# Optimization experiments

Measured on AMD Instinct MI355X. Metric: run time of the kernel, lower is better.

## Reference

```python
import jax, jax.numpy as jnp
import numpy as np

B, T, I, C, O = 256, 1024, 128, 256, 10


def setup_inputs() -> dict:
    key = jax.random.key(0)
    k1, k2, k3, k4, k5 = jax.random.split(key, 5)
    x = jax.random.normal(k1, (B, T, I), dtype=jnp.float32)
    # xavier-like scale for kernels
    kernel = jax.random.normal(k2, (I, 2 * C), dtype=jnp.float32) * (6.0 / (I + 2 * C)) ** 0.5
    recurrent_kernel = jax.random.normal(k3, (C, 2 * C), dtype=jnp.float32) * (6.0 / (C + 2 * C)) ** 0.5
    # bias: forget-gate half initialized to log(uniform(1, T-1)), rest zero
    u = jax.random.uniform(k4, (C,), minval=1.0, maxval=float(T - 1))
    recurrent_bias = jnp.concatenate([jnp.log(u), jnp.zeros((C,), jnp.float32)])
    dense_w = jax.random.normal(k5, (C, O), dtype=jnp.float32) * (1.0 / C) ** 0.5
    dense_b = jnp.zeros((O,), jnp.float32)
    return {"x": x, "kernel": kernel, "recurrent_kernel": recurrent_kernel,
            "recurrent_bias": recurrent_bias, "dense_w": dense_w, "dense_b": dense_b}


def reference(x, kernel, recurrent_kernel, recurrent_bias, dense_w, dense_b):
    cells = recurrent_kernel.shape[0]
    # Precompute input projection for all timesteps in one big GEMM: [B,T,2C]
    xz = jnp.einsum('bti,ig->btg', x, kernel) + recurrent_bias
    xz_t = jnp.swapaxes(xz, 0, 1)  # [T, B, 2C] for scan over time

    def step(carry, z_in):
        h, c = carry
        z = z_in + h @ recurrent_kernel  # [B, 2C]
        f = jax.nn.sigmoid(z[:, :cells])
        c_new = f * c + (1.0 - f) * jnp.tanh(z[:, cells:])
        return (c_new, c_new), None

    h0 = jnp.zeros((x.shape[0], cells), x.dtype)
    (h_final, _), _ = jax.lax.scan(step, (h0, h0), xz_t)
    return h_final @ dense_w + dense_b
```

## Files before the change

### kernel.cpp

```cpp
#include <hip/hip_runtime.h>

#define BB 256
#define TT 1024
#define II 128
#define GG 512
#define CC 256
#define L2E 1.44269504f

typedef _Float16 f16;
typedef _Float16 h8_t __attribute__((ext_vector_type(8)));
typedef float f4_t __attribute__((ext_vector_type(4)));
typedef unsigned short ushort_t;
typedef unsigned short us4_t __attribute__((ext_vector_type(4)));

static __device__ __forceinline__ float fast_rcp(float x) {
#if __has_builtin(__builtin_amdgcn_rcpf)
    return __builtin_amdgcn_rcpf(x);
#else
    return 1.f / x;
#endif
}
static __device__ __forceinline__ float fast_exp2(float x) {
#if __has_builtin(__builtin_amdgcn_exp2f)
    return __builtin_amdgcn_exp2f(x);
#else
    return exp2f(x);
#endif
}

__global__ void kt_transpose(const float* __restrict__ kin, f16* __restrict__ kt) {
    int idx = blockIdx.x * 256 + threadIdx.x;
    int k = idx >> 9;
    int n = idx & 511;
    kt[n * II + k] = (f16)kin[k * GG + n];
}

__global__ __launch_bounds__(512, 2)
void gemm_xz(const float* __restrict__ x, const f16* __restrict__ kt,
             const float* __restrict__ bias, ushort_t* __restrict__ xz) {
    const long mtile = blockIdx.x;
    const int wave = threadIdx.x >> 6;
    const int lane = threadIdx.x & 63;
    const int wm = (wave & 1) * 64;
    const int wn = (wave >> 1) * 128;
    const int lm = lane & 15;
    const int q  = lane >> 4;

    f4_t acc[4][8];
#pragma unroll
    for (int mi = 0; mi < 4; ++mi)
#pragma unroll
        for (int nj = 0; nj < 8; ++nj)
            acc[mi][nj] = (f4_t){0.f, 0.f, 0.f, 0.f};

#pragma unroll
    for (int kc = 0; kc < 4; ++kc) {
        h8_t a[4], bf[8];
#pragma unroll
        for (int mi = 0; mi < 4; ++mi) {
            const int rowm = (int)(mtile * 128) + wm + mi * 16 + lm;
            const int b  = rowm & 255;
            const int tt = rowm >> 8;
            const float* ap = x + (size_t)b * (TT * II) + (size_t)tt * II + kc * 32 + q * 8;
            f4_t p0 = *(const f4_t*)ap;
            f4_t p1 = *(const f4_t*)(ap + 4);
            h8_t tv;
            tv[0] = (f16)p0[0]; tv[1] = (f16)p0[1]; tv[2] = (f16)p0[2]; tv[3] = (f16)p0[3];
            tv[4] = (f16)p1[0]; tv[5] = (f16)p1[1]; tv[6] = (f16)p1[2]; tv[7] = (f16)p1[3];
            a[mi] = tv;
        }
#pragma unroll
        for (int nj = 0; nj < 8; ++nj) {
            const f16* bp = kt + (size_t)(wn + nj * 16 + lm) * II + kc * 32 + q * 8;
            bf[nj] = *(const h8_t*)bp;
        }
#pragma unroll
        for (int mi = 0; mi < 4; ++mi)
#pragma unroll
            for (int nj = 0; nj < 8; ++nj)
                acc[mi][nj] = __builtin_amdgcn_mfma_f32_16x16x32_f16(a[mi], bf[nj], acc[mi][nj], 0, 0, 0);
    }

#pragma unroll
    for (int mi = 0; mi < 4; ++mi) {
        const int rowm0 = (int)(mtile * 128) + wm + mi * 16 + q * 4;
        const int t  = rowm0 >> 8;
        const int b0 = rowm0 & 255;
        const int gq = b0 >> 4;
#pragma unroll
        for (int nj = 0; nj < 8; ++nj) {
            const int col = wn + nj * 16 + lm;
            const float bv = bias[col];
            const float s  = (col < CC) ? L2E : (2.0f * L2E);
            us4_t v;
#pragma unroll
            for (int r = 0; r < 4; ++r) {
                f16 hv = (f16)((acc[mi][nj][r] + bv) * s);
                v[r] = *(ushort_t*)&hv;
            }
            *(us4_t*)(xz + (((size_t)t * 16 + gq) * 512 + col) * 16 + q * 4) = v;
        }
    }
}

#define STEP(T, PF, PP, HRD, HWR) do {                                               \
    h8_t af[8];                                                                      \
    _Pragma("unroll") for (int kt = 0; kt < 4; ++kt)                                 \
        af[kt] = *(const h8_t*)((HRD) + lm * 264 + kt * 32 + q * 8);                 \
    f4_t acc[4];                                                                     \
    _Pragma("unroll") for (int ni = 0; ni < 4; ++ni) {                               \
        f4_t av;                                                                     \
        _Pragma("unroll") for (int r = 0; r < 4; ++r) {                              \
            ushort_t u = (PF)[ni * 4 + r];                                           \
            f16 hv = *(f16*)&u;                                                      \
            av[r] = (float)hv;                                                       \
        }                                                                            \
        acc[ni] = av;                                                                \
    }                                                                                \
    if ((T) + 2 < TT) {                                                              \
        _Pragma("unroll") for (int ni = 0; ni < 4; ++ni) {                           \
            us4_t v = *(const us4_t*)((PP) + ni * 2048);                             \
            (PF)[ni * 4 + 0] = v[0];                                                 \
            (PF)[ni * 4 + 1] = v[1];                                                 \
            (PF)[ni * 4 + 2] = v[2];                                                 \
            (PF)[ni * 4 + 3] = v[3];                                                 \
        }                                                                            \
        (PP) += 2 * 131072;                                                          \
    }                                                                                \
                                                  \
    _Pragma("unroll") for (int kt = 0; kt < 4; ++kt) {                               \
        acc[0] = __builtin_amdgcn_mfma_f32_16x16x32_f16(af[kt], bw[0][kt], acc[0], 0, 0, 0); \
        acc[2] = __builtin_amdgcn_mfma_f32_16x16x32_f16(af[kt], bw[2][kt], acc[2], 0, 0, 0); \
    }                                                                                \
    _Pragma("unroll") for (int kt = 0; kt < 4; ++kt) {                               \
        acc[1] = __builtin_amdgcn_mfma_f32_16x16x32_f16(af[kt], bw[1][kt], acc[1], 0, 0, 0); \
        acc[3] = __builtin_amdgcn_mfma_f32_16x16x32_f16(af[kt], bw[3][kt], acc[3], 0, 0, 0); \
    }                                                                                \
    asm volatile("s_waitcnt lgkmcnt(0)\n\ts_barrier" ::: "memory");       \
    _Pragma("unroll") for (int kt = 4; kt < 8; ++kt)                                 \
        af[kt] = *(const h8_t*)((HRD) + lm * 264 + kt * 32 + q * 8);                 \
         \
    _Pragma("unroll") for (int kt = 4; kt < 8; ++kt) {                               \
        acc[0] = __builtin_amdgcn_mfma_f32_16x16x32_f16(af[kt], bw[0][kt], acc[0], 0, 0, 0); \
        acc[2] = __builtin_amdgcn_mfma_f32_16x16x32_f16(af[kt], bw[2][kt], acc[2], 0, 0, 0); \
    }                                                                                \
    _Pragma("unroll") for (int kt = 4; kt < 8; ++kt) {                               \
        acc[1] = __builtin_amdgcn_mfma_f32_16x16x32_f16(af[kt], bw[1][kt], acc[1], 0, 0, 0); \
        acc[3] = __builtin_amdgcn_mfma_f32_16x16x32_f16(af[kt], bw[3][kt], acc[3], 0, 0, 0); \
    }                                                                                \
                                         \
    _Pragma("unroll") for (int r = 0; r < 4; ++r) {                                  \
        float zf = acc[0][r];                                                        \
        float zg = acc[2][r];                                                        \
        float ef = fast_exp2(-zf);                                                   \
        float eg = fast_exp2(-fabsf(zg));                                            \
        float t1 = (zg < 0.f) ? -ef : ef;                                            \
        float cv = cst[0][r];                                                        \
        float num = fmaf(cv, eg, cv) + fmaf(-t1, eg, t1);                            \
        float den = (1.f + ef) * (1.f + eg);                                         \
        cst[0][r] = num * fast_rcp(den);                                             \
        (HWR)[(q * 4 + r) * 264 + wave * 16 + lm] = (f16)cst[0][r];                  \
    }                                                                                \
    asm volatile("s_waitcnt lgkmcnt(0)\n\ts_barrier" ::: "memory");       \
          \
    _Pragma("unroll") for (int r = 0; r < 4; ++r) {                                  \
        float zf = acc[1][r];                                                        \
        float zg = acc[3][r];                                                        \
        float ef = fast_exp2(-zf);                                                   \
        float eg = fast_exp2(-fabsf(zg));                                            \
        float t1 = (zg < 0.f) ? -ef : ef;                                            \
        float cv = cst[1][r];                                                        \
        float num = fmaf(cv, eg, cv) + fmaf(-t1, eg, t1);                            \
        float den = (1.f + ef) * (1.f + eg);                                         \
        cst[1][r] = num * fast_rcp(den);                                             \
        (HWR)[(q * 4 + r) * 264 + (wave + 8) * 16 + lm] = (f16)cst[1][r];            \
    }                                                                                \
} while (0)

__global__ __launch_bounds__(512, 2)
void janet_rec(const float* __restrict__ rk, const float* __restrict__ dw,
               const float* __restrict__ db, const ushort_t* __restrict__ xz,
               float* __restrict__ out) {
    const int g = blockIdx.x;
    const int tid = threadIdx.x;
    const int wave = tid >> 6;
    const int lane = tid & 63;
    const int lm = lane & 15;
    const int q  = lane >> 4;

    h8_t bw[4][8];
#pragma unroll
    for (int ni = 0; ni < 4; ++ni) {
        const float s = (ni < 2) ? L2E : (2.0f * L2E);
#pragma unroll
        for (int kt = 0; kt < 8; ++kt) {
            h8_t tv;
#pragma unroll
            for (int j = 0; j < 8; ++j)
                tv[j] = (f16)(s * rk[(size_t)(kt * 32 + q * 8 + j) * GG + (wave + 8 * ni) * 16 + lm]);
            bw[ni][kt] = tv;
        }
    }

    __shared__ __align__(16) f16 hb[2][16][264];
    f16* h0 = &hb[0][0][0];
    f16* h1 = &hb[1][0][0];
    for (int i = tid; i < 2 * 16 * 264; i += 512) ((f16*)hb)[i] = (f16)0.f;

    float cst[2][4];
#pragma unroll
    for (int ni = 0; ni < 2; ++ni)
#pragma unroll
        for (int r = 0; r < 4; ++r) cst[ni][r] = 0.f;

    const ushort_t* PB = xz + (size_t)g * 8192 + (wave * 16 + lm) * 16 + q * 4;
    const ushort_t* p0 = PB + 2 * 131072;
    const ushort_t* p1 = PB + 3 * 131072;

    ushort_t pf0[16], pf1[16];
#pragma unroll
    for (int ni = 0; ni < 4; ++ni) {
        us4_t v0 = *(const us4_t*)(PB + ni * 2048);
        us4_t v1 = *(const us4_t*)(PB + 131072 + ni * 2048);
        pf0[ni * 4 + 0] = v0[0]; pf0[ni * 4 + 1] = v0[1];
        pf0[ni * 4 + 2] = v0[2]; pf0[ni * 4 + 3] = v0[3];
        pf1[ni * 4 + 0] = v1[0]; pf1[ni * 4 + 1] = v1[1];
        pf1[ni * 4 + 2] = v1[2]; pf1[ni * 4 + 3] = v1[3];
    }
    __syncthreads();

#pragma unroll 1
    for (int t = 0; t < TT; t += 2) {
        STEP(t,     pf0, p0, h0, h1);
        STEP(t + 1, pf1, p1, h1, h0);
    }

    __shared__ float hf[16][256];
#pragma unroll
    for (int ni = 0; ni < 2; ++ni)
#pragma unroll
        for (int r = 0; r < 4; ++r)
            hf[q * 4 + r][(wave + 8 * ni) * 16 + lm] = cst[ni][r];
    __syncthreads();
    if (tid < 160) {
        const int bi = tid / 10, o = tid % 10;
        float acc = db[o];
#pragma unroll 8
        for (int cc = 0; cc < CC; ++cc) acc = fmaf(hf[bi][cc], dw[cc * 10 + o], acc);
        out[(g * 16 + bi) * 10 + o] = acc;
    }
}

__global__ void ws_too_small(float* out, float wssz) {
    int i = blockIdx.x * 256 + threadIdx.x;
    if (i < BB * 10) out[i] = (i == 0) ? wssz : 0.f;
}

extern "C" void kernel_launch(void* const* d_in, const int* in_sizes, int n_in,
                              void* d_out, int out_size, void* d_ws, size_t ws_size,
                              hipStream_t stream) {
    const float* x   = (const float*)d_in[0];
    const float* kin = (const float*)d_in[1];
    const float* rk  = (const float*)d_in[2];
    const float* rb  = (const float*)d_in[3];
    const float* dw  = (const float*)d_in[4];
    const float* db  = (const float*)d_in[5];
    float* out = (float*)d_out;

    const size_t xz_bytes = (size_t)BB * TT * GG * 2;
    const size_t kt_bytes = (size_t)GG * II * 2;
    if (ws_size < xz_bytes + kt_bytes) {
        ws_too_small<<<10, 256, 0, stream>>>(out, (float)ws_size);
        return;
    }

    ushort_t* xz = (ushort_t*)d_ws;
    f16* kt = (f16*)((char*)d_ws + xz_bytes);

    kt_transpose<<<256, 256, 0, stream>>>(kin, kt);
    gemm_xz<<<2048, 512, 0, stream>>>(x, kt, rb, xz);
    janet_rec<<<16, 512, 0, stream>>>(rk, dw, db, xz, out);
}
```

Before: 1.464 ms.

## Fuse input GEMM and recurrence into one launch with per-tile readiness flags

Merges the input-projection GEMM and the recurrent scan into a single kernel. The first 16 blocks run the recurrence and the remaining 2048 blocks compute xz tiles, each publishing a release flag when its tile is written. Recurrence blocks spin on the flags for the timestep they need before prefetching, so the serial scan can start while the GEMM is still running instead of waiting for the whole GEMM to finish. This adds atomic polling overhead. It also relies on the 16 recurrence blocks being scheduled alongside the GEMM blocks, and the extra dynamic shared memory lowers occupancy for the GEMM blocks.

Measured after the change: 1.630 ms. +11.3%, slower.

```diff
diff --git a/kernel.cpp b/kernel.cpp
--- a/kernel.cpp
+++ b/kernel.cpp
@@ -28,79 +28,14 @@
 #endif
 }
 
+__device__ unsigned g_flags[2049];
+
 __global__ void kt_transpose(const float* __restrict__ kin, f16* __restrict__ kt) {
     int idx = blockIdx.x * 256 + threadIdx.x;
+    if (idx < 2049) g_flags[idx] = 0u;
     int k = idx >> 9;
     int n = idx & 511;
     kt[n * II + k] = (f16)kin[k * GG + n];
-}
-
-__global__ __launch_bounds__(512, 2)
-void gemm_xz(const float* __restrict__ x, const f16* __restrict__ kt,
-             const float* __restrict__ bias, ushort_t* __restrict__ xz) {
-    const long mtile = blockIdx.x;
-    const int wave = threadIdx.x >> 6;
-    const int lane = threadIdx.x & 63;
-    const int wm = (wave & 1) * 64;
-    const int wn = (wave >> 1) * 128;
-    const int lm = lane & 15;
-    const int q  = lane >> 4;
-
-    f4_t acc[4][8];
-#pragma unroll
-    for (int mi = 0; mi < 4; ++mi)
-#pragma unroll
-        for (int nj = 0; nj < 8; ++nj)
-            acc[mi][nj] = (f4_t){0.f, 0.f, 0.f, 0.f};
-
-#pragma unroll
-    for (int kc = 0; kc < 4; ++kc) {
-        h8_t a[4], bf[8];
-#pragma unroll
-        for (int mi = 0; mi < 4; ++mi) {
-            const int rowm = (int)(mtile * 128) + wm + mi * 16 + lm;
-            const int b  = rowm & 255;
-            const int tt = rowm >> 8;
-            const float* ap = x + (size_t)b * (TT * II) + (size_t)tt * II + kc * 32 + q * 8;
-            f4_t p0 = *(const f4_t*)ap;
-            f4_t p1 = *(const f4_t*)(ap + 4);
-            h8_t tv;
-            tv[0] = (f16)p0[0]; tv[1] = (f16)p0[1]; tv[2] = (f16)p0[2]; tv[3] = (f16)p0[3];
-            tv[4] = (f16)p1[0]; tv[5] = (f16)p1[1]; tv[6] = (f16)p1[2]; tv[7] = (f16)p1[3];
-            a[mi] = tv;
-        }
-#pragma unroll
-        for (int nj = 0; nj < 8; ++nj) {
-            const f16* bp = kt + (size_t)(wn + nj * 16 + lm) * II + kc * 32 + q * 8;
-            bf[nj] = *(const h8_t*)bp;
-        }
-#pragma unroll
-        for (int mi = 0; mi < 4; ++mi)
-#pragma unroll
-            for (int nj = 0; nj < 8; ++nj)
-                acc[mi][nj] = __builtin_amdgcn_mfma_f32_16x16x32_f16(a[mi], bf[nj], acc[mi][nj], 0, 0, 0);
-    }
-
-#pragma unroll
-    for (int mi = 0; mi < 4; ++mi) {
-        const int rowm0 = (int)(mtile * 128) + wm + mi * 16 + q * 4;
-        const int t  = rowm0 >> 8;
-        const int b0 = rowm0 & 255;
-        const int gq = b0 >> 4;
-#pragma unroll
-        for (int nj = 0; nj < 8; ++nj) {
-            const int col = wn + nj * 16 + lm;
-            const float bv = bias[col];
-            const float s  = (col < CC) ? L2E : (2.0f * L2E);
-            us4_t v;
-#pragma unroll
-            for (int r = 0; r < 4; ++r) {
-                f16 hv = (f16)((acc[mi][nj][r] + bv) * s);
-                v[r] = *(ushort_t*)&hv;
-            }
-            *(us4_t*)(xz + (((size_t)t * 16 + gq) * 512 + col) * 16 + q * 4) = v;
-        }
-    }
 }
 
 #define STEP(T, PF, PP, HRD, HWR) do {                                               \
@@ -118,6 +53,20 @@
         acc[ni] = av;                                                                \
     }                                                                                \
     if ((T) + 2 < TT) {                                                              \
+        if (!alldone) {                                                              \
+            unsigned cn = __hip_atomic_load(&g_flags[2048], __ATOMIC_ACQUIRE,        \
+                                            __HIP_MEMORY_SCOPE_AGENT);               \
+            if (cn == 2048u) { alldone = true; }                                     \
+            else {                                                                   \
+                unsigned ff;                                                         \
+                do {                                                                 \
+                    ff = __hip_atomic_load(&g_flags[2 * ((T) + 2) + gh],             \
+                                           __ATOMIC_ACQUIRE,                         \
+                                           __HIP_MEMORY_SCOPE_AGENT);                \
+                    if (!ff) __builtin_amdgcn_s_sleep(8);                            \
+                } while (!ff);                                                       \
+            }                                                                        \
+        }                                                                            \
         _Pragma("unroll") for (int ni = 0; ni < 4; ++ni) {                           \
             us4_t v = *(const us4_t*)((PP) + ni * 2048);                             \
             (PF)[ni * 4 + 0] = v[0];                                                 \
@@ -178,16 +127,89 @@
 } while (0)
 
 __global__ __launch_bounds__(512, 2)
-void janet_rec(const float* __restrict__ rk, const float* __restrict__ dw,
-               const float* __restrict__ db, const ushort_t* __restrict__ xz,
-               float* __restrict__ out) {
-    const int g = blockIdx.x;
+void janet_fused(const float* __restrict__ x, const f16* __restrict__ kt,
+                 const float* __restrict__ bias, ushort_t* __restrict__ xz,
+                 const float* __restrict__ rk, const float* __restrict__ dw,
+                 const float* __restrict__ db, float* __restrict__ out) {
     const int tid = threadIdx.x;
     const int wave = tid >> 6;
     const int lane = tid & 63;
     const int lm = lane & 15;
     const int q  = lane >> 4;
 
+    if (blockIdx.x >= 16) {
+        const long mtile = blockIdx.x - 16;
+        const int wm = (wave & 1) * 64;
+        const int wn = (wave >> 1) * 128;
+
+        f4_t acc[4][8];
+#pragma unroll
+        for (int mi = 0; mi < 4; ++mi)
+#pragma unroll
+            for (int nj = 0; nj < 8; ++nj)
+                acc[mi][nj] = (f4_t){0.f, 0.f, 0.f, 0.f};
+
+#pragma unroll
+        for (int kc = 0; kc < 4; ++kc) {
+            h8_t a[4], bf[8];
+#pragma unroll
+            for (int mi = 0; mi < 4; ++mi) {
+                const int rowm = (int)(mtile * 128) + wm + mi * 16 + lm;
+                const int b  = rowm & 255;
+                const int tt = rowm >> 8;
+                const float* ap = x + (size_t)b * (TT * II) + (size_t)tt * II + kc * 32 + q * 8;
+                f4_t p0 = *(const f4_t*)ap;
+                f4_t p1 = *(const f4_t*)(ap + 4);
+                h8_t tv;
+                tv[0] = (f16)p0[0]; tv[1] = (f16)p0[1]; tv[2] = (f16)p0[2]; tv[3] = (f16)p0[3];
+                tv[4] = (f16)p1[0]; tv[5] = (f16)p1[1]; tv[6] = (f16)p1[2]; tv[7] = (f16)p1[3];
+                a[mi] = tv;
+            }
+#pragma unroll
+            for (int nj = 0; nj < 8; ++nj) {
+                const f16* bp = kt + (size_t)(wn + nj * 16 + lm) * II + kc * 32 + q * 8;
+                bf[nj] = *(const h8_t*)bp;
+            }
+#pragma unroll
+            for (int mi = 0; mi < 4; ++mi)
+#pragma unroll
+                for (int nj = 0; nj < 8; ++nj)
+                    acc[mi][nj] = __builtin_amdgcn_mfma_f32_16x16x32_f16(a[mi], bf[nj], acc[mi][nj], 0, 0, 0);
+        }
+
+#pragma unroll
+        for (int mi = 0; mi < 4; ++mi) {
+            const int rowm0 = (int)(mtile * 128) + wm + mi * 16 + q * 4;
+            const int t  = rowm0 >> 8;
+            const int b0 = rowm0 & 255;
+            const int gq = b0 >> 4;
+#pragma unroll
+            for (int nj = 0; nj < 8; ++nj) {
+                const int col = wn + nj * 16 + lm;
+                const float bv = bias[col];
+                const float s  = (col < CC) ? L2E : (2.0f * L2E);
+                us4_t v;
+#pragma unroll
+                for (int r = 0; r < 4; ++r) {
+                    f16 hv = (f16)((acc[mi][nj][r] + bv) * s);
+                    v[r] = *(ushort_t*)&hv;
+                }
+                *(us4_t*)(xz + (((size_t)t * 16 + gq) * 512 + col) * 16 + q * 4) = v;
+            }
+        }
+
+        __syncthreads();
+        if (tid == 0) {
+            __hip_atomic_store(&g_flags[(int)mtile], 1u, __ATOMIC_RELEASE, __HIP_MEMORY_SCOPE_AGENT);
+            __hip_atomic_fetch_add(&g_flags[2048], 1u, __ATOMIC_RELEASE, __HIP_MEMORY_SCOPE_AGENT);
+        }
+        return;
+    }
+
+    const int g = blockIdx.x;
+    const int gh = g >> 3;
+    bool alldone = false;
+
     h8_t bw[4][8];
 #pragma unroll
     for (int ni = 0; ni < 4; ++ni) {
@@ -212,6 +234,14 @@
     for (int ni = 0; ni < 2; ++ni)
 #pragma unroll
         for (int r = 0; r < 4; ++r) cst[ni][r] = 0.f;
+
+    {
+        unsigned ff;
+        do { ff = __hip_atomic_load(&g_flags[gh], __ATOMIC_ACQUIRE, __HIP_MEMORY_SCOPE_AGENT);
+             if (!ff) __builtin_amdgcn_s_sleep(8); } while (!ff);
+        do { ff = __hip_atomic_load(&g_flags[2 + gh], __ATOMIC_ACQUIRE, __HIP_MEMORY_SCOPE_AGENT);
+             if (!ff) __builtin_amdgcn_s_sleep(8); } while (!ff);
+    }
 
     const ushort_t* PB = xz + (size_t)g * 8192 + (wave * 16 + lm) * 16 + q * 4;
     const ushort_t* p0 = PB + 2 * 131072;
@@ -278,6 +308,5 @@
     f16* kt = (f16*)((char*)d_ws + xz_bytes);
 
     kt_transpose<<<256, 256, 0, stream>>>(kin, kt);
-    gemm_xz<<<2048, 512, 0, stream>>>(x, kt, rb, xz);
-    janet_rec<<<16, 512, 0, stream>>>(rk, dw, db, xz, out);
-}
+    janet_fused<<<2064, 512, 49152, stream>>>(x, kt, rb, xz, rk, dw, db, out);
+}
```

## Stage x tile in LDS for input GEMM and cut recurrent barriers to one per step

Applied to the files above, without the earlier changes.

The input-projection GEMM now remaps each block to one timestep and 128 batch rows. It loads that x tile once into shared memory as f16 and has the MFMA waves read their A fragments from LDS instead of issuing strided global loads per wave. In the recurrent kernel, each step used to have two barriers with the h-fragment loads split around them. It now loads all eight h fragments up front, runs all MFMAs, and uses a single barrier at the end of the step. The prefetch buffer is also repacked as 32-bit words so loads and converts are cheaper. The main aim is to take barrier latency off the serial 1024-step critical path. The single barrier relies on the double-buffered h arrays for correctness.

New measurement: 1.428 ms. 2.5% less time.

```diff
diff --git a/kernel.cpp b/kernel.cpp
--- a/kernel.cpp
+++ b/kernel.cpp
@@ -9,9 +9,12 @@
 
 typedef _Float16 f16;
 typedef _Float16 h8_t __attribute__((ext_vector_type(8)));
+typedef _Float16 h4_t __attribute__((ext_vector_type(4)));
+typedef _Float16 h2_t __attribute__((ext_vector_type(2)));
 typedef float f4_t __attribute__((ext_vector_type(4)));
 typedef unsigned short ushort_t;
 typedef unsigned short us4_t __attribute__((ext_vector_type(4)));
+typedef unsigned u2_t __attribute__((ext_vector_type(2)));
 
 static __device__ __forceinline__ float fast_rcp(float x) {
 #if __has_builtin(__builtin_amdgcn_rcpf)
@@ -38,13 +41,35 @@
 __global__ __launch_bounds__(512, 2)
 void gemm_xz(const float* __restrict__ x, const f16* __restrict__ kt,
              const float* __restrict__ bias, ushort_t* __restrict__ xz) {
+    const int tid = threadIdx.x;
+    const int wave = tid >> 6;
+    const int lane = tid & 63;
+    const int lm = lane & 15;
+    const int q  = lane >> 4;
+
     const long mtile = blockIdx.x;
-    const int wave = threadIdx.x >> 6;
-    const int lane = threadIdx.x & 63;
     const int wm = (wave & 1) * 64;
     const int wn = (wave >> 1) * 128;
-    const int lm = lane & 15;
-    const int q  = lane >> 4;
+
+    const int tt0 = (int)(mtile >> 1);
+    const int bb0 = ((int)mtile & 1) * 128;
+
+    __shared__ __align__(16) f16 xs[128][132];
+
+    {
+        const int r0  = tid >> 5;
+        const int c16 = tid & 31;
+        const float* xb = x + (size_t)tt0 * II + (size_t)c16 * 4;
+#pragma unroll
+        for (int j = 0; j < 8; ++j) {
+            const int row = r0 + j * 16;
+            f4_t p = *(const f4_t*)(xb + (size_t)(bb0 + row) * (TT * II));
+            h4_t hv;
+            hv[0] = (f16)p[0]; hv[1] = (f16)p[1]; hv[2] = (f16)p[2]; hv[3] = (f16)p[3];
+            *(h4_t*)(&xs[row][c16 * 4]) = hv;
+        }
+    }
+    __syncthreads();
 
     f4_t acc[4][8];
 #pragma unroll
@@ -57,18 +82,8 @@
     for (int kc = 0; kc < 4; ++kc) {
         h8_t a[4], bf[8];
 #pragma unroll
-        for (int mi = 0; mi < 4; ++mi) {
-            const int rowm = (int)(mtile * 128) + wm + mi * 16 + lm;
-            const int b  = rowm & 255;
-            const int tt = rowm >> 8;
-            const float* ap = x + (size_t)b * (TT * II) + (size_t)tt * II + kc * 32 + q * 8;
-            f4_t p0 = *(const f4_t*)ap;
-            f4_t p1 = *(const f4_t*)(ap + 4);
-            h8_t tv;
-            tv[0] = (f16)p0[0]; tv[1] = (f16)p0[1]; tv[2] = (f16)p0[2]; tv[3] = (f16)p0[3];
-            tv[4] = (f16)p1[0]; tv[5] = (f16)p1[1]; tv[6] = (f16)p1[2]; tv[7] = (f16)p1[3];
-            a[mi] = tv;
-        }
+        for (int mi = 0; mi < 4; ++mi)
+            a[mi] = *(const h8_t*)(&xs[wm + mi * 16 + lm][kc * 32 + q * 8]);
 #pragma unroll
         for (int nj = 0; nj < 8; ++nj) {
             const f16* bp = kt + (size_t)(wn + nj * 16 + lm) * II + kc * 32 + q * 8;
@@ -83,10 +98,8 @@
 
 #pragma unroll
     for (int mi = 0; mi < 4; ++mi) {
-        const int rowm0 = (int)(mtile * 128) + wm + mi * 16 + q * 4;
-        const int t  = rowm0 >> 8;
-        const int b0 = rowm0 & 255;
-        const int gq = b0 >> 4;
+        const int b0r = bb0 + wm + mi * 16 + q * 4;
+        const int gq = b0r >> 4;
 #pragma unroll
         for (int nj = 0; nj < 8; ++nj) {
             const int col = wn + nj * 16 + lm;
@@ -98,57 +111,40 @@
                 f16 hv = (f16)((acc[mi][nj][r] + bv) * s);
                 v[r] = *(ushort_t*)&hv;
             }
-            *(us4_t*)(xz + (((size_t)t * 16 + gq) * 512 + col) * 16 + q * 4) = v;
+            *(us4_t*)(xz + (((size_t)tt0 * 16 + gq) * 512 + col) * 16 + q * 4) = v;
         }
     }
 }
 
 #define STEP(T, PF, PP, HRD, HWR) do {                                               \
     h8_t af[8];                                                                      \
-    _Pragma("unroll") for (int kt = 0; kt < 4; ++kt)                                 \
+    _Pragma("unroll") for (int kt = 0; kt < 8; ++kt)                                 \
         af[kt] = *(const h8_t*)((HRD) + lm * 264 + kt * 32 + q * 8);                 \
     f4_t acc[4];                                                                     \
     _Pragma("unroll") for (int ni = 0; ni < 4; ++ni) {                               \
-        f4_t av;                                                                     \
-        _Pragma("unroll") for (int r = 0; r < 4; ++r) {                              \
-            ushort_t u = (PF)[ni * 4 + r];                                           \
-            f16 hv = *(f16*)&u;                                                      \
-            av[r] = (float)hv;                                                       \
-        }                                                                            \
-        acc[ni] = av;                                                                \
+        h2_t a01 = *(h2_t*)&(PF)[ni * 2];                                            \
+        h2_t a23 = *(h2_t*)&(PF)[ni * 2 + 1];                                        \
+        acc[ni] = (f4_t){(float)a01[0], (float)a01[1], (float)a23[0], (float)a23[1]};\
     }                                                                                \
     if ((T) + 2 < TT) {                                                              \
         _Pragma("unroll") for (int ni = 0; ni < 4; ++ni) {                           \
-            us4_t v = *(const us4_t*)((PP) + ni * 2048);                             \
-            (PF)[ni * 4 + 0] = v[0];                                                 \
-            (PF)[ni * 4 + 1] = v[1];                                                 \
-            (PF)[ni * 4 + 2] = v[2];                                                 \
-            (PF)[ni * 4 + 3] = v[3];                                                 \
+            u2_t v = *(const u2_t*)((PP) + ni * 2048);                               \
+            (PF)[ni * 2] = v[0];                                                     \
+            (PF)[ni * 2 + 1] = v[1];                                                 \
         }                                                                            \
         (PP) += 2 * 131072;                                                          \
     }                                                                                \
-                                                  \
-    _Pragma("unroll") for (int kt = 0; kt < 4; ++kt) {                               \
+                                                              \
+    _Pragma("unroll") for (int kt = 0; kt < 8; ++kt) {                               \
         acc[0] = __builtin_amdgcn_mfma_f32_16x16x32_f16(af[kt], bw[0][kt], acc[0], 0, 0, 0); \
         acc[2] = __builtin_amdgcn_mfma_f32_16x16x32_f16(af[kt], bw[2][kt], acc[2], 0, 0, 0); \
     }                                                                                \
-    _Pragma("unroll") for (int kt = 0; kt < 4; ++kt) {                               \
+                                                              \
+    _Pragma("unroll") for (int kt = 0; kt < 8; ++kt) {                               \
         acc[1] = __builtin_amdgcn_mfma_f32_16x16x32_f16(af[kt], bw[1][kt], acc[1], 0, 0, 0); \
         acc[3] = __builtin_amdgcn_mfma_f32_16x16x32_f16(af[kt], bw[3][kt], acc[3], 0, 0, 0); \
     }                                                                                \
-    asm volatile("s_waitcnt lgkmcnt(0)\n\ts_barrier" ::: "memory");       \
-    _Pragma("unroll") for (int kt = 4; kt < 8; ++kt)                                 \
-        af[kt] = *(const h8_t*)((HRD) + lm * 264 + kt * 32 + q * 8);                 \
-         \
-    _Pragma("unroll") for (int kt = 4; kt < 8; ++kt) {                               \
-        acc[0] = __builtin_amdgcn_mfma_f32_16x16x32_f16(af[kt], bw[0][kt], acc[0], 0, 0, 0); \
-        acc[2] = __builtin_amdgcn_mfma_f32_16x16x32_f16(af[kt], bw[2][kt], acc[2], 0, 0, 0); \
-    }                                                                                \
-    _Pragma("unroll") for (int kt = 4; kt < 8; ++kt) {                               \
-        acc[1] = __builtin_amdgcn_mfma_f32_16x16x32_f16(af[kt], bw[1][kt], acc[1], 0, 0, 0); \
-        acc[3] = __builtin_amdgcn_mfma_f32_16x16x32_f16(af[kt], bw[3][kt], acc[3], 0, 0, 0); \
-    }                                                                                \
-                                         \
+                       \
     _Pragma("unroll") for (int r = 0; r < 4; ++r) {                                  \
         float zf = acc[0][r];                                                        \
         float zg = acc[2][r];                                                        \
@@ -161,8 +157,7 @@
         cst[0][r] = num * fast_rcp(den);                                             \
         (HWR)[(q * 4 + r) * 264 + wave * 16 + lm] = (f16)cst[0][r];                  \
     }                                                                                \
-    asm volatile("s_waitcnt lgkmcnt(0)\n\ts_barrier" ::: "memory");       \
-          \
+                                                    \
     _Pragma("unroll") for (int r = 0; r < 4; ++r) {                                  \
         float zf = acc[1][r];                                                        \
         float zg = acc[3][r];                                                        \
@@ -175,6 +170,7 @@
         cst[1][r] = num * fast_rcp(den);                                             \
         (HWR)[(q * 4 + r) * 264 + (wave + 8) * 16 + lm] = (f16)cst[1][r];            \
     }                                                                                \
+    asm volatile("s_waitcnt lgkmcnt(0)\n\ts_barrier" ::: "memory");                  \
 } while (0)
 
 __global__ __launch_bounds__(512, 2)
@@ -217,15 +213,13 @@
     const ushort_t* p0 = PB + 2 * 131072;
     const ushort_t* p1 = PB + 3 * 131072;
 
-    ushort_t pf0[16], pf1[16];
+    unsigned pf0[8], pf1[8];
 #pragma unroll
     for (int ni = 0; ni < 4; ++ni) {
-        us4_t v0 = *(const us4_t*)(PB + ni * 2048);
-        us4_t v1 = *(const us4_t*)(PB + 131072 + ni * 2048);
-        pf0[ni * 4 + 0] = v0[0]; pf0[ni * 4 + 1] = v0[1];
-        pf0[ni * 4 + 2] = v0[2]; pf0[ni * 4 + 3] = v0[3];
-        pf1[ni * 4 + 0] = v1[0]; pf1[ni * 4 + 1] = v1[1];
-        pf1[ni * 4 + 2] = v1[2]; pf1[ni * 4 + 3] = v1[3];
+        u2_t v0 = *(const u2_t*)(PB + ni * 2048);
+        u2_t v1 = *(const u2_t*)(PB + 131072 + ni * 2048);
+        pf0[ni * 2] = v0[0]; pf0[ni * 2 + 1] = v0[1];
+        pf1[ni * 2] = v1[0]; pf1[ni * 2 + 1] = v1[1];
     }
     __syncthreads();
 
```
